# Optimization experiments

Measured on AMD Instinct MI355X. Metric: run time of the kernel, lower is better.

Reference implementation:

```python
import math
import jax, jax.numpy as jnp
import numpy as np

N_FFT = 1024
HOP = 320
WIN = 800
SR = 32000
N_MELS = 128
FMIN = 0.0
FMAX = SR / 2.0
NUM_BINS = N_FFT // 2 + 1  # 513
PREEMPH = 0.97


def _hann_window(n):
    # torch.hann_window(n, periodic=False): 0.5 - 0.5*cos(2*pi*i/(n-1))
    i = np.arange(n, dtype=np.float64)
    return (0.5 - 0.5 * np.cos(2.0 * np.pi * i / (n - 1))).astype(np.float32)


def _fourier_basis():
    offset = (N_FFT - WIN) // 2
    win_full = np.zeros(N_FFT, dtype=np.float64)
    win_full[offset:offset + WIN] = _hann_window(WIN)
    n = np.arange(N_FFT, dtype=np.float64)[None, :]
    k = np.arange(NUM_BINS, dtype=np.float64)[:, None]
    ang = 2.0 * np.pi * k * (n / float(N_FFT))
    cos_k = np.cos(ang) * win_full
    sin_k = -np.sin(ang) * win_full
    return np.concatenate([cos_k, sin_k], axis=0).astype(np.float32)  # [2*513, 1024]


def _kaldi_mel_banks():
    # torchaudio.compliance.kaldi.get_mel_banks with vtln_warp_factor=1.0
    num_fft_bins = N_FFT // 2
    fft_bin_width = SR / float(N_FFT)
    mel = lambda f: 1127.0 * np.log(1.0 + f / 700.0)
    mel_low, mel_high = mel(FMIN), mel(FMAX)
    delta = (mel_high - mel_low) / (N_MELS + 1)
    left = mel_low + np.arange(N_MELS, dtype=np.float64) * delta  # [M]
    right = left + 2.0 * delta
    freqs = fft_bin_width * np.arange(num_fft_bins, dtype=np.float64)
    m = mel(freqs)[None, :]  # [1, 512]
    up = (m - left[:, None]) / delta
    down = (right[:, None] - m) / delta
    bank = np.maximum(0.0, np.minimum(up, down))  # [128, 512]
    bank = np.pad(bank, ((0, 0), (0, 1)))  # pad one zero column -> [128, 513]
    return bank.astype(np.float32)


def setup_inputs() -> dict:
    key = jax.random.key(0)
    x = jax.random.normal(key, (32, 320000), dtype=jnp.float32)
    return {
        "x": x,
        "fourier_basis": jnp.asarray(_fourier_basis()),
        "mel_basis": jnp.asarray(_kaldi_mel_banks()),
    }


def reference(x, fourier_basis, mel_basis):
    # preemphasis: conv1d with kernel [-0.97, 1.0] (cross-correlation)
    y = x[:, 1:] - PREEMPH * x[:, :-1]  # [B, T-1]
    # center pad by n_fft//2
    pad = N_FFT // 2
    y = jnp.pad(y, ((0, 0), (pad, pad)))
    Tp = y.shape[1]
    frames = (Tp - N_FFT) // HOP + 1
    # frame extraction: [B, frames, n_fft]
    idx = jnp.arange(frames)[:, None] * HOP + jnp.arange(N_FFT)[None, :]
    f = y[:, idx]
    # explicit DFT via dense matmul: [B, 2*num_bins, frames]
    spec = jnp.einsum('btn,cn->bct', f, fourier_basis)
    real = spec[:, :NUM_BINS, :]
    imag = spec[:, NUM_BINS:, :]
    power = real * real + imag * imag  # [B, num_bins, frames]
    mel = jnp.einsum('mf,bft->bmt', mel_basis, power)
    log_mel = (jnp.log(mel + 1e-05) + 4.5) / 5.0
    return log_mel
```

## Files before the change

### kernel.cpp

```cpp
#include <hip/hip_runtime.h>
#include <math.h>

typedef _Float16 half8 __attribute__((ext_vector_type(8)));
typedef float f32x4 __attribute__((ext_vector_type(4)));

constexpr int kNFFT    = 1024;
constexpr int kHop     = 320;
constexpr int kMels    = 128;
constexpr int kFrames  = 1000;
constexpr int kBatch   = 32;
constexpr int kXLen    = 320000;
constexpr int kYLen    = kXLen - 1;
constexpr int kYPad    = 328704;
constexpr int kYOff    = 512;
constexpr float kPre   = 0.97f;
constexpr int kPStride = 544;
constexpr int kKsLo    = 3;
constexpr int kKsHi    = 28;

constexpr size_t kYLvl     = (size_t)kBatch * kYPad;
constexpr size_t kFragLvl  = 64ull * 32 * 64 * 8;
constexpr size_t kFragOff  = 2 * kYLvl;
constexpr size_t kMelFrOff = kFragOff + 2 * kFragLvl;
constexpr size_t kMelFrSz  = 8ull * 17 * 64 * 8;
constexpr size_t kPowOff   = kMelFrOff + kMelFrSz;

constexpr int kYJobBlks   = (kYPad / 8 + 255) / 256;
constexpr int kYJobTotal  = kYJobBlks * kBatch;
constexpr int kFragBlks   = 131072 / 256;
constexpr int kMelBlks    = (8 * 17 * 64) / 256;
constexpr int kPrepGrid   = kYJobTotal + kFragBlks + kMelBlks;

__global__ void prep_all(const float* __restrict__ x, const float* __restrict__ basis,
                         const float* __restrict__ melb, _Float16* __restrict__ ws) {
    _Float16* ypad  = ws;
    _Float16* fr    = ws + kFragOff;
    _Float16* melfr = ws + kMelFrOff;
    const int bid = blockIdx.x;
    const int tid = threadIdx.x;

    if (bid < kYJobTotal) {
        int b = bid / kYJobBlks;
        int blk = bid - b * kYJobBlks;
        int e0 = (blk * 256 + tid) * 8;
        if (e0 >= kYPad) return;
        const float* xb = x + (size_t)b * kXLen;
        int yi = e0 - kYOff;
        float v[8];
        if (yi >= 0 && yi <= kXLen - 9) {
            float4 A = *(const float4*)(xb + yi);
            float4 B = *(const float4*)(xb + yi + 4);
            float C = xb[yi + 8];
            v[0] = A.y - kPre * A.x;  v[1] = A.z - kPre * A.y;
            v[2] = A.w - kPre * A.z;  v[3] = B.x - kPre * A.w;
            v[4] = B.y - kPre * B.x;  v[5] = B.z - kPre * B.y;
            v[6] = B.w - kPre * B.z;  v[7] = C   - kPre * B.w;
        } else {
            #pragma unroll
            for (int j = 0; j < 8; ++j) {
                int g = yi + j;
                v[j] = (g >= 0 && g < kYLen) ? xb[g + 1] - kPre * xb[g] : 0.0f;
            }
        }
        half8 hv, mv;
        #pragma unroll
        for (int j = 0; j < 8; ++j) {
            _Float16 h = (_Float16)v[j];
            hv[j] = h;
            mv[j] = (_Float16)(v[j] - (float)h);
        }
        size_t idx = (size_t)b * kYPad + e0;
        *(half8*)(ypad + idx) = hv;
        *(half8*)(ypad + idx + kYLvl) = mv;
    } else if (bid < kYJobTotal + kFragBlks) {
        int id = (bid - kYJobTotal) * 256 + tid;
        int L  = id & 63;
        int ks = (id >> 6) & 31;
        int g  = id >> 11;
        int r  = 16 * g + (L & 15);
        int orig = (r <= 512) ? r : r + 1;
        const float* src = basis + (size_t)orig * kNFFT + 32 * ks + (L >> 4) * 8;
        float4 s0 = *(const float4*)(src);
        float4 s1 = *(const float4*)(src + 4);
        float a[8] = {s0.x, s0.y, s0.z, s0.w, s1.x, s1.y, s1.z, s1.w};
        half8 hv, mv;
        #pragma unroll
        for (int j = 0; j < 8; ++j) {
            _Float16 h = (_Float16)a[j];
            hv[j] = h;
            mv[j] = (_Float16)(a[j] - (float)h);
        }
        _Float16* dst = fr + (size_t)id * 8;
        *(half8*)dst = hv;
        *(half8*)(dst + kFragLvl) = mv;
    } else {
        int id = (bid - kYJobTotal - kFragBlks) * 256 + tid;
        if (id >= 8 * 17 * 64) return;
        int f = id / 1088;
        int rem = id - f * 1088;
        int ks = rem >> 6;
        int L = rem & 63;
        int m = 16 * f + (L & 15);
        int kb = 32 * ks + (L >> 4) * 8;
        half8 hv;
        #pragma unroll
        for (int j = 0; j < 8; ++j) {
            int k = kb + j;
            hv[j] = (k < 513) ? (_Float16)melb[(size_t)m * 513 + k] : (_Float16)0.0f;
        }
        *(half8*)(melfr + (size_t)id * 8) = hv;
    }
}

__global__ __launch_bounds__(256, 2)
void stft_power(const _Float16* __restrict__ frags,
                const _Float16* __restrict__ ypad,
                _Float16* __restrict__ pw) {
    __shared__ __align__(16) _Float16 ash[2][16 * 512];
    const int tid  = threadIdx.x;
    const int w    = tid >> 6;
    const int lane = tid & 63;
    const int quad = lane >> 4;
    const int l16  = lane & 15;
    const int nt = blockIdx.x, g = blockIdx.y, b = blockIdx.z;
    const int t0 = nt * 256 + w * 64;
    const _Float16* yb0 = ypad + (size_t)b * kYPad;
    const _Float16* yb1 = yb0 + kYLvl;

    f32x4 acc[8][4] = {};

    auto stageA = [&](int ks, int pbuf) {
        #pragma unroll
        for (int c = 0; c < 4; ++c) {
            int slot = w + 4 * c;
            int f = slot & 7, lv = slot >> 3;
            int Gf = (f < 4) ? (4 * g + f) : (32 + 4 * g + (f - 4));
            const _Float16* gp = frags + (size_t)lv * kFragLvl
                               + ((size_t)(Gf * 32 + ks) * 64 + lane) * 8;
            __builtin_amdgcn_global_load_lds(
                (const __attribute__((address_space(1))) void*)gp,
                (__attribute__((address_space(3))) void*)&ash[pbuf][slot * 512],
                16, 0, 0);
        }
    };
    auto loadB2 = [&](int ks, int nf0, half8* bh, half8* bm) {
        #pragma unroll
        for (int nf = nf0; nf < nf0 + 2; ++nf) {
            int off = (t0 + nf * 16 + l16) * kHop + ks * 32 + quad * 8;
            bh[nf] = *(const half8*)(yb0 + off);
            bm[nf] = *(const half8*)(yb1 + off);
        }
    };
    auto mfma2 = [&](int f0, half8 h0, half8 m0, half8 h1, half8 m1,
                     half8* bh, half8* bm) {
        #pragma unroll
        for (int nf = 0; nf < 4; ++nf) {
            f32x4 a = acc[f0][nf];
            a = __builtin_amdgcn_mfma_f32_16x16x32_f16(h0, bh[nf], a, 0, 0, 0);
            a = __builtin_amdgcn_mfma_f32_16x16x32_f16(m0, bh[nf], a, 0, 0, 0);
            a = __builtin_amdgcn_mfma_f32_16x16x32_f16(h0, bm[nf], a, 0, 0, 0);
            acc[f0][nf] = a;
            f32x4 c = acc[f0 + 1][nf];
            c = __builtin_amdgcn_mfma_f32_16x16x32_f16(h1, bh[nf], c, 0, 0, 0);
            c = __builtin_amdgcn_mfma_f32_16x16x32_f16(m1, bh[nf], c, 0, 0, 0);
            c = __builtin_amdgcn_mfma_f32_16x16x32_f16(h1, bm[nf], c, 0, 0, 0);
            acc[f0 + 1][nf] = c;
        }
    };

    auto step = [&](int ks, int pbuf, half8* bhC, half8* bmC,
                    half8* bhN, half8* bmN, bool next) {
        #pragma unroll
        for (int p = 0; p < 4; ++p) {
            const int f0 = 2 * p;
            half8 h0 = *(const half8*)&ash[pbuf][f0 * 512 + lane * 8];
            half8 m0 = *(const half8*)&ash[pbuf][(8 + f0) * 512 + lane * 8];
            half8 h1 = *(const half8*)&ash[pbuf][(f0 + 1) * 512 + lane * 8];
            half8 m1 = *(const half8*)&ash[pbuf][(9 + f0) * 512 + lane * 8];
            if (p == 0 && next) stageA(ks + 1, pbuf ^ 1);
            if (p == 1 && next) loadB2(ks + 1, 0, bhN, bmN);
            if (p == 2 && next) loadB2(ks + 1, 2, bhN, bmN);
            if (p == 3)
                asm volatile("s_waitcnt vmcnt(8)" ::: "memory");
            __builtin_amdgcn_s_barrier();
            __builtin_amdgcn_s_setprio(1);
            mfma2(f0, h0, m0, h1, m1, bhC, bmC);
            __builtin_amdgcn_s_setprio(0);
            __builtin_amdgcn_s_barrier();
        }
    };

    half8 bhA[4], bmA[4], bhB[4], bmB[4];
    stageA(kKsLo, 0);
    loadB2(kKsLo, 0, bhA, bmA);
    loadB2(kKsLo, 2, bhA, bmA);
    asm volatile("s_waitcnt vmcnt(0)" ::: "memory");
    __builtin_amdgcn_s_barrier();

    for (int kss = 0; kss < 13; ++kss) {
        int ks = kKsLo + 2 * kss;
        step(ks,     0, bhA, bmA, bhB, bmB, true);
        step(ks + 1, 1, bhB, bmB, bhA, bmA, kss < 12);
    }

    #pragma unroll
    for (int mf = 0; mf < 4; ++mf) {
        int b0 = 64 * g + 16 * mf + 4 * quad;
        #pragma unroll
        for (int nf = 0; nf < 4; ++nf) {
            int t = t0 + nf * 16 + l16;
            size_t row = ((size_t)((b << 10) + t)) * kPStride;
            struct alignas(8) h4 { _Float16 v[4]; } pp;
            #pragma unroll
            for (int rr = 0; rr < 4; ++rr) {
                float pA = acc[mf][nf][rr];
                float pB = acc[4 + mf][nf][rr];
                float p2 = pA * pA + pB * pB;
                if (g == 0 && mf == 0 && quad == 0 && rr == 0) {
                    p2 = pA * pA;
                    pw[row + 512] = (_Float16)(pB * pB);
                }
                pp.v[rr] = (_Float16)p2;
            }
            *(decltype(pp)*)&pw[row + b0] = pp;
        }
    }
}

__global__ __launch_bounds__(512)
void mel_mfma(const _Float16* __restrict__ melfr, const _Float16* __restrict__ pw,
              float* __restrict__ out) {
    __shared__ __align__(16) _Float16 psh[64 * 576];
    const int tid  = threadIdx.x;
    const int w    = tid >> 6;
    const int lane = tid & 63;
    const int quad = lane >> 4;
    const int l16  = lane & 15;
    const int tw   = w & 3;
    const int mh   = w >> 2;
    const int nt = blockIdx.x, b = blockIdx.y;
    const int t0 = nt * 64;

    for (int c = tid; c < 64 * 68; c += 512) {
        int row = c / 68;
        int col = c - row * 68;
        *(half8*)&psh[row * 576 + ((col ^ (row & 7)) << 3)] =
            *(const half8*)(pw + ((size_t)((b << 10) + t0 + row)) * kPStride + col * 8);
    }
    __syncthreads();

    const int t = t0 + tw * 16 + l16;
    const int lrow = tw * 16 + l16;
    const int rkey = lrow & 7;
    f32x4 acc[4] = {};
    const _Float16* mfr0 = melfr + ((size_t)(mh * 4) * 17 * 64 + lane) * 8;
    #pragma unroll
    for (int ks = 0; ks < 17; ++ks) {
        half8 bp = *(const half8*)&psh[lrow * 576 + (((4 * ks + quad) ^ rkey) << 3)];
        #pragma unroll
        for (int f = 0; f < 4; ++f) {
            half8 af = *(const half8*)(mfr0 + (size_t)(f * 17 + ks) * 64 * 8);
            acc[f] = __builtin_amdgcn_mfma_f32_16x16x32_f16(af, bp, acc[f], 0, 0, 0);
        }
    }
    if (t < kFrames) {
        #pragma unroll
        for (int f = 0; f < 4; ++f) {
            #pragma unroll
            for (int r = 0; r < 4; ++r) {
                int m = mh * 64 + 16 * f + 4 * quad + r;
                out[((size_t)(b * kMels + m)) * kFrames + t] =
                    (__logf(acc[f][r] + 1e-5f) + 4.5f) * 0.2f;
            }
        }
    }
}

extern "C" void kernel_launch(void* const* d_in, const int* in_sizes, int n_in,
                              void* d_out, int out_size, void* d_ws, size_t ws_size,
                              hipStream_t stream) {
    const float* x     = (const float*)d_in[0];
    const float* basis = (const float*)d_in[1];
    const float* melb  = (const float*)d_in[2];
    float* out = (float*)d_out;

    _Float16* ws    = (_Float16*)d_ws;
    _Float16* frags = ws + kFragOff;
    _Float16* melfr = ws + kMelFrOff;
    _Float16* pw    = ws + kPowOff;

    prep_all<<<dim3(kPrepGrid), 256, 0, stream>>>(x, basis, melb, ws);
    stft_power<<<dim3(4, 8, kBatch), 256, 0, stream>>>(frags, ws, pw);
    mel_mfma<<<dim3(16, kBatch), 512, 0, stream>>>(melfr, pw, out);
}
```

Measured before the change: 240.1 us.

## Fuse preemphasis and fp16 split into STFT kernel, drop padded signal buffer

The preemphasis filter, center padding and hi/lo fp16 split now happen inside the STFT MFMA kernel, which reads raw fp32 x directly. The prep kernel no longer writes two padded fp16 copies of the signal to global memory, removing that write and its later re-read. In exchange, each of the 8 frequency-group blocks redoes the conversion for its frames, loads are fp32 and therefore twice as wide, and the pipeline now waits with vmcnt(0) instead of vmcnt(8) before the conversion step, which may expose more load latency.

```diff
diff --git a/kernel.cpp b/kernel.cpp
--- a/kernel.cpp
+++ b/kernel.cpp
@@ -11,69 +11,31 @@
 constexpr int kBatch   = 32;
 constexpr int kXLen    = 320000;
 constexpr int kYLen    = kXLen - 1;
-constexpr int kYPad    = 328704;
 constexpr int kYOff    = 512;
 constexpr float kPre   = 0.97f;
 constexpr int kPStride = 544;
 constexpr int kKsLo    = 3;
 constexpr int kKsHi    = 28;
 
-constexpr size_t kYLvl     = (size_t)kBatch * kYPad;
 constexpr size_t kFragLvl  = 64ull * 32 * 64 * 8;
-constexpr size_t kFragOff  = 2 * kYLvl;
+constexpr size_t kFragOff  = 2ull * kBatch * 328704;
 constexpr size_t kMelFrOff = kFragOff + 2 * kFragLvl;
 constexpr size_t kMelFrSz  = 8ull * 17 * 64 * 8;
 constexpr size_t kPowOff   = kMelFrOff + kMelFrSz;
 
-constexpr int kYJobBlks   = (kYPad / 8 + 255) / 256;
-constexpr int kYJobTotal  = kYJobBlks * kBatch;
 constexpr int kFragBlks   = 131072 / 256;
 constexpr int kMelBlks    = (8 * 17 * 64) / 256;
-constexpr int kPrepGrid   = kYJobTotal + kFragBlks + kMelBlks;
+constexpr int kPrepGrid   = kFragBlks + kMelBlks;
 
 __global__ void prep_all(const float* __restrict__ x, const float* __restrict__ basis,
                          const float* __restrict__ melb, _Float16* __restrict__ ws) {
-    _Float16* ypad  = ws;
     _Float16* fr    = ws + kFragOff;
     _Float16* melfr = ws + kMelFrOff;
     const int bid = blockIdx.x;
     const int tid = threadIdx.x;
 
-    if (bid < kYJobTotal) {
-        int b = bid / kYJobBlks;
-        int blk = bid - b * kYJobBlks;
-        int e0 = (blk * 256 + tid) * 8;
-        if (e0 >= kYPad) return;
-        const float* xb = x + (size_t)b * kXLen;
-        int yi = e0 - kYOff;
-        float v[8];
-        if (yi >= 0 && yi <= kXLen - 9) {
-            float4 A = *(const float4*)(xb + yi);
-            float4 B = *(const float4*)(xb + yi + 4);
-            float C = xb[yi + 8];
-            v[0] = A.y - kPre * A.x;  v[1] = A.z - kPre * A.y;
-            v[2] = A.w - kPre * A.z;  v[3] = B.x - kPre * A.w;
-            v[4] = B.y - kPre * B.x;  v[5] = B.z - kPre * B.y;
-            v[6] = B.w - kPre * B.z;  v[7] = C   - kPre * B.w;
-        } else {
-            #pragma unroll
-            for (int j = 0; j < 8; ++j) {
-                int g = yi + j;
-                v[j] = (g >= 0 && g < kYLen) ? xb[g + 1] - kPre * xb[g] : 0.0f;
-            }
-        }
-        half8 hv, mv;
-        #pragma unroll
-        for (int j = 0; j < 8; ++j) {
-            _Float16 h = (_Float16)v[j];
-            hv[j] = h;
-            mv[j] = (_Float16)(v[j] - (float)h);
-        }
-        size_t idx = (size_t)b * kYPad + e0;
-        *(half8*)(ypad + idx) = hv;
-        *(half8*)(ypad + idx + kYLvl) = mv;
-    } else if (bid < kYJobTotal + kFragBlks) {
-        int id = (bid - kYJobTotal) * 256 + tid;
+    if (bid < kFragBlks) {
+        int id = bid * 256 + tid;
         int L  = id & 63;
         int ks = (id >> 6) & 31;
         int g  = id >> 11;
@@ -94,7 +56,7 @@
         *(half8*)dst = hv;
         *(half8*)(dst + kFragLvl) = mv;
     } else {
-        int id = (bid - kYJobTotal - kFragBlks) * 256 + tid;
+        int id = (bid - kFragBlks) * 256 + tid;
         if (id >= 8 * 17 * 64) return;
         int f = id / 1088;
         int rem = id - f * 1088;
@@ -114,7 +76,7 @@
 
 __global__ __launch_bounds__(256, 2)
 void stft_power(const _Float16* __restrict__ frags,
-                const _Float16* __restrict__ ypad,
+                const float* __restrict__ x,
                 _Float16* __restrict__ pw) {
     __shared__ __align__(16) _Float16 ash[2][16 * 512];
     const int tid  = threadIdx.x;
@@ -124,11 +86,18 @@
     const int l16  = lane & 15;
     const int nt = blockIdx.x, g = blockIdx.y, b = blockIdx.z;
     const int t0 = nt * 256 + w * 64;
-    const _Float16* yb0 = ypad + (size_t)b * kYPad;
-    const _Float16* yb1 = yb0 + kYLvl;
+    const float* xb = x + (size_t)b * kXLen;
 
     f32x4 acc[8][4] = {};
-
+    float4 XA[4], XB[4];
+    float  XC[4];
+    half8  bh[4], bm[4];
+
+    auto dirtyW = [&](int ks) {
+        int offmin = t0 * kHop + ks * 32;
+        int offmax = (t0 + 63) * kHop + ks * 32 + 24;
+        return (offmin < kYOff) || (offmax - kYOff > kXLen - 16);
+    };
     auto stageA = [&](int ks, int pbuf) {
         #pragma unroll
         for (int c = 0; c < 4; ++c) {
@@ -143,16 +112,46 @@
                 16, 0, 0);
         }
     };
-    auto loadB2 = [&](int ks, int nf0, half8* bh, half8* bm) {
+    auto loadX = [&](int ks, int nf0) {
+        bool dirty = dirtyW(ks);
         #pragma unroll
         for (int nf = nf0; nf < nf0 + 2; ++nf) {
-            int off = (t0 + nf * 16 + l16) * kHop + ks * 32 + quad * 8;
-            bh[nf] = *(const half8*)(yb0 + off);
-            bm[nf] = *(const half8*)(yb1 + off);
-        }
-    };
-    auto mfma2 = [&](int f0, half8 h0, half8 m0, half8 h1, half8 m1,
-                     half8* bh, half8* bm) {
+            int yi = (t0 + nf * 16 + l16) * kHop + ks * 32 + quad * 8 - kYOff;
+            if (!dirty) {
+                XA[nf] = *(const float4*)(xb + yi);
+                XB[nf] = *(const float4*)(xb + yi + 4);
+                XC[nf] = xb[yi + 8];
+            } else {
+                bool ld8 = (yi >= 0) && (yi <= kXLen - 8);
+                if (ld8) {
+                    XA[nf] = *(const float4*)(xb + yi);
+                    XB[nf] = *(const float4*)(xb + yi + 4);
+                } else {
+                    XA[nf] = float4{0.f, 0.f, 0.f, 0.f};
+                    XB[nf] = float4{0.f, 0.f, 0.f, 0.f};
+                }
+                XC[nf] = (yi >= 0 && yi + 8 < kXLen) ? xb[yi + 8] : 0.f;
+            }
+        }
+    };
+    auto convX = [&](int ks) {
+        bool dirty = dirtyW(ks);
+        #pragma unroll
+        for (int nf = 0; nf < 4; ++nf) {
+            float xx[9] = {XA[nf].x, XA[nf].y, XA[nf].z, XA[nf].w,
+                           XB[nf].x, XB[nf].y, XB[nf].z, XB[nf].w, XC[nf]};
+            int yi = (t0 + nf * 16 + l16) * kHop + ks * 32 + quad * 8 - kYOff;
+            #pragma unroll
+            for (int j = 0; j < 8; ++j) {
+                float v = xx[j + 1] - kPre * xx[j];
+                if (dirty) v = (yi + j < kYLen) ? v : 0.f;
+                _Float16 h = (_Float16)v;
+                bh[nf][j] = h;
+                bm[nf][j] = (_Float16)(v - (float)h);
+            }
+        }
+    };
+    auto mfma2 = [&](int f0, half8 h0, half8 m0, half8 h1, half8 m1) {
         #pragma unroll
         for (int nf = 0; nf < 4; ++nf) {
             f32x4 a = acc[f0][nf];
@@ -168,8 +167,7 @@
         }
     };
 
-    auto step = [&](int ks, int pbuf, half8* bhC, half8* bmC,
-                    half8* bhN, half8* bmN, bool next) {
+    auto step = [&](int ks, int pbuf, bool next) {
         #pragma unroll
         for (int p = 0; p < 4; ++p) {
             const int f0 = 2 * p;
@@ -178,29 +176,30 @@
             half8 h1 = *(const half8*)&ash[pbuf][(f0 + 1) * 512 + lane * 8];
             half8 m1 = *(const half8*)&ash[pbuf][(9 + f0) * 512 + lane * 8];
             if (p == 0 && next) stageA(ks + 1, pbuf ^ 1);
-            if (p == 1 && next) loadB2(ks + 1, 0, bhN, bmN);
-            if (p == 2 && next) loadB2(ks + 1, 2, bhN, bmN);
+            if (p == 1 && next) loadX(ks + 1, 0);
+            if (p == 2 && next) loadX(ks + 1, 2);
             if (p == 3)
-                asm volatile("s_waitcnt vmcnt(8)" ::: "memory");
+                asm volatile("s_waitcnt vmcnt(0)" ::: "memory");
             __builtin_amdgcn_s_barrier();
             __builtin_amdgcn_s_setprio(1);
-            mfma2(f0, h0, m0, h1, m1, bhC, bmC);
+            mfma2(f0, h0, m0, h1, m1);
             __builtin_amdgcn_s_setprio(0);
+            if (p == 3 && next) convX(ks + 1);
             __builtin_amdgcn_s_barrier();
         }
     };
 
-    half8 bhA[4], bmA[4], bhB[4], bmB[4];
     stageA(kKsLo, 0);
-    loadB2(kKsLo, 0, bhA, bmA);
-    loadB2(kKsLo, 2, bhA, bmA);
+    loadX(kKsLo, 0);
+    loadX(kKsLo, 2);
     asm volatile("s_waitcnt vmcnt(0)" ::: "memory");
+    convX(kKsLo);
     __builtin_amdgcn_s_barrier();
 
     for (int kss = 0; kss < 13; ++kss) {
         int ks = kKsLo + 2 * kss;
-        step(ks,     0, bhA, bmA, bhB, bmB, true);
-        step(ks + 1, 1, bhB, bmB, bhA, bmA, kss < 12);
+        step(ks,     0, true);
+        step(ks + 1, 1, kss < 12);
     }
 
     #pragma unroll
@@ -290,6 +289,6 @@
     _Float16* pw    = ws + kPowOff;
 
     prep_all<<<dim3(kPrepGrid), 256, 0, stream>>>(x, basis, melb, ws);
-    stft_power<<<dim3(4, 8, kBatch), 256, 0, stream>>>(frags, ws, pw);
+    stft_power<<<dim3(4, 8, kBatch), 256, 0, stream>>>(frags, x, pw);
     mel_mfma<<<dim3(16, kBatch), 512, 0, stream>>>(melfr, pw, out);
 }
```

Measured after the change: 342.2 us. +42.5%, slower.
